# Kernel optimization log

Measured on AMD Instinct MI355X. Metric: run time of the kernel, lower is better.

The kernel has to match this reference:

```python
import jax, jax.numpy as jnp
import numpy as np
from jax import lax

NUM_LAYERS = 8
K = 3
C = 128  # residual/gate/skip channels
DIL_H = (1, 2, 4, 8, 1, 2, 4, 8)
DIL_W = (1, 2, 4, 8, 16, 32, 64, 128)
DN = ('NCHW', 'OIHW', 'NCHW')


def _conv(x, w, b, dh=1, dw=1, pad_h=0, pad_w=0):
    # causal along H: pad only on top by pad_h (equivalent to pytorch's
    # symmetric pad + out[:, :, :-pad_h] slice); symmetric along W.
    out = lax.conv_general_dilated(
        x, w, window_strides=(1, 1),
        padding=((pad_h, 0), (pad_w, pad_w)),
        rhs_dilation=(dh, dw), dimension_numbers=DN)
    return out + b[None, :, None, None]


def setup_inputs() -> dict:
    key = jax.random.key(0)
    ks = jax.random.split(key, 6)
    B, H, W = 2, 16, 4096
    return {
        'x': jax.random.normal(ks[0], (B, 1, H, W), jnp.float32),
        'c': jax.random.normal(ks[1], (B, 80, H, W), jnp.float32),
        'front_w': jax.random.normal(ks[2], (C, 1, 1, 1), jnp.float32),
        'front_b': jnp.zeros((C,), jnp.float32),
        'fg_w': jax.random.normal(ks[3], (NUM_LAYERS, 2 * C, C, K, K), jnp.float32) * (1.0 / np.sqrt(C * K * K)),
        'fg_b': jnp.zeros((NUM_LAYERS, 2 * C), jnp.float32),
        'fgc_w': jax.random.normal(ks[4], (NUM_LAYERS, 2 * C, 80, 1, 1), jnp.float32) * (1.0 / np.sqrt(80)),
        'fgc_b': jnp.zeros((NUM_LAYERS, 2 * C), jnp.float32),
        'rs_w': jax.random.normal(ks[5], (NUM_LAYERS, 2 * C, C, 1, 1), jnp.float32) * (1.0 / np.sqrt(C)),
        'rs_b': jnp.zeros((NUM_LAYERS, 2 * C), jnp.float32),
    }


def reference(x, c, front_w, front_b, fg_w, fg_b, fgc_w, fgc_b, rs_w, rs_b):
    # front 1x1 conv (causal but pad_h = 0 for kernel_size=1)
    h = _conv(x, front_w, front_b)  # [B, C, H, W]
    skip = jnp.zeros_like(h)
    for i in range(NUM_LAYERS):
        dh, dw = DIL_H[i], DIL_W[i]
        pad_h = dh * (K - 1)
        pad_w = dw * (K - 1) // 2
        # dilated causal conv -> [B, 2C, H, W]
        hg = _conv(h, fg_w[i], fg_b[i], dh, dw, pad_h, pad_w)
        # 1x1 conditioning conv on c
        cg = _conv(c, fgc_w[i], fgc_b[i])
        a = hg + cg
        acts = jnp.tanh(a[:, :C]) * jax.nn.sigmoid(a[:, C:])
        # 1x1 res/skip conv -> [B, 2C, H, W]
        rs = _conv(acts, rs_w[i], rs_b[i])
        h = h + rs[:, :C]
        skip = skip + rs[:, C:]
    return skip
```

## Files before the change

kernel.cpp:

```cpp
#include <hip/hip_runtime.h>
#include <math.h>

#define NL    8
#define CCH   128
#define CINC  80
#define CPAD  128
#define HH    16
#define WW    4096
#define HW    (HH*WW)
#define PADW  128
#define WWP   (WW + 2*PADW)
#define NT    10
#define PADF  64

#define HBF_N   (2*HH*WWP*CCH)
#define ZROW_N  (WWP*CCH)
#define CT_N    (2*HW*CPAD)
#define SKB_N   (2*HW*CCH)
#define GW_N    (NL*NT*4*16*64*8)
#define RW_N    (NL*4*16*64*8)

using v8s   = __attribute__((ext_vector_type(8))) short;
using f32x4 = __attribute__((ext_vector_type(4))) float;

__device__ __forceinline__ unsigned short f2bf(float f) {
    unsigned int u = __builtin_bit_cast(unsigned int, f);
    u += 0x7fffu + ((u >> 16) & 1u);
    return (unsigned short)(u >> 16);
}
__device__ __forceinline__ float bfu2f(unsigned int v) {
    return __builtin_bit_cast(float, v << 16);
}
__device__ __forceinline__ float gated(float a, float g) {
    float ac = fminf(a, 15.0f);
    float e  = __expf(2.0f * ac);
    float th = (e - 1.0f) * __builtin_amdgcn_rcpf(e + 1.0f);
    float sg = __builtin_amdgcn_rcpf(1.0f + __expf(-g));
    return th * sg;
}

__device__ __forceinline__ void gl_lds16(const void* g, void* l) {
    __builtin_amdgcn_global_load_lds(
        (const __attribute__((address_space(1))) unsigned int*)g,
        (__attribute__((address_space(3))) unsigned int*)l, 16, 0, 0);
}

__device__ __host__ __forceinline__ int tap_of(int t) { return (t < 7) ? t : (t == 8 ? 8 : 7); }

__global__ void prep_weights(const float* __restrict__ fg_w, const float* __restrict__ fgc_w,
                             const float* __restrict__ rs_w,
                             const float* __restrict__ fg_b, const float* __restrict__ fgc_b,
                             const float* __restrict__ rs_b,
                             unsigned short* __restrict__ gw, unsigned short* __restrict__ rw,
                             float* __restrict__ gbias, float* __restrict__ rbias) {
    const int total = GW_N + RW_N + 2 * NL * 256;
    const int stride = gridDim.x * blockDim.x;
    for (int idx = blockIdx.x * blockDim.x + threadIdx.x; idx < total; idx += stride) {
        if (idx < GW_N) {
            int t0 = idx;
            int j = t0 & 7;  t0 >>= 3;
            int l = t0 & 63; t0 >>= 6;
            int mt = t0 & 15; t0 >>= 4;
            int tq = t0 % (NT*4);
            int i  = t0 / (NT*4);
            int t  = tq >> 2, q = tq & 3;
            int m  = mt*16 + (l & 15);
            int oo = (m & 1)*128 + (m >> 1);
            int ci = q*32 + 8*(l >> 4) + j;
            float v;
            if (t == 7) {
                v = (ci < CINC) ? fgc_w[((size_t)i*256 + oo)*CINC + ci] : 0.0f;
            } else {
                int tt = tap_of(t);
                v = fg_w[(((size_t)i*256 + oo)*128 + ci)*9 + tt];
            }
            gw[idx] = f2bf(v);
        } else if (idx < GW_N + RW_N) {
            int t0 = idx - GW_N;
            int j = t0 & 7;  t0 >>= 3;
            int l = t0 & 63; t0 >>= 6;
            int mt = t0 & 15; t0 >>= 4;
            int q = t0 & 3;
            int i = t0 >> 2;
            int m  = mt*16 + (l & 15);
            int oo = (m & 1)*128 + (m >> 1);
            int ci = q*32 + 8*(l >> 4) + j;
            rw[idx - GW_N] = f2bf(rs_w[((size_t)i*256 + oo)*128 + ci]);
        } else {
            int t0 = idx - GW_N - RW_N;
            if (t0 < NL*256) {
                int i = t0 >> 8, m = t0 & 255;
                int oo = (m & 1)*128 + (m >> 1);
                gbias[t0] = fg_b[i*256 + oo] + fgc_b[i*256 + oo];
            } else {
                t0 -= NL*256;
                int i = t0 >> 8, m = t0 & 255;
                int oo = (m & 1)*128 + (m >> 1);
                rbias[t0] = rs_b[i*256 + oo];
            }
        }
    }
}

__global__ void front_kernel(const float* __restrict__ xsrc,
                             const float* __restrict__ fw, const float* __restrict__ fb,
                             unsigned short* __restrict__ hbf0,
                             unsigned short* __restrict__ hbf1, unsigned short* __restrict__ zrow) {
    const int stride = gridDim.x * blockDim.x;
    const int t0 = blockIdx.x * blockDim.x + threadIdx.x;
    for (int idx = t0; idx < HBF_N; idx += stride) {
        int c = idx & 127;
        int rest = idx >> 7;
        int xp = rest % WWP; rest /= WWP;
        int y = rest & 15;
        int b = rest >> 4;
        int x = xp - PADW;
        if (x >= 0 && x < WW)
            hbf0[idx] = f2bf(fw[c] * xsrc[((size_t)(b*HH + y))*WW + x] + fb[c]);
        else
            hbf0[idx] = 0;
    }
    const int PADN = 2*HH*2*PADW*CCH;
    for (int idx = t0; idx < PADN; idx += stride) {
        int c = idx & 127;
        int r = idx >> 7;
        int xo = r % (2*PADW); r /= (2*PADW);
        int y = r & 15;
        int b = r >> 4;
        int xp = (xo < PADW) ? xo : xo + WW;
        hbf1[(((size_t)(b*HH + y))*WWP + xp)*CCH + c] = 0;
    }
    for (int idx = t0; idx < ZROW_N; idx += stride) zrow[idx] = 0;
}

__global__ __launch_bounds__(256) void cond_transpose(const float* __restrict__ cin,
                                                      unsigned short* __restrict__ cT) {
    __shared__ unsigned short lt[CINC][72];
    const int tid = threadIdx.x, lane = tid & 63, w = tid >> 6;
    const int x0 = blockIdx.x * 64, y = blockIdx.y, b = blockIdx.z;
#pragma unroll
    for (int r = 0; r < 20; ++r) {
        int ci = w*20 + r;
        float v = cin[(((size_t)(b*CINC + ci))*HH + y)*WW + x0 + lane];
        lt[ci][lane] = f2bf(v);
    }
    __syncthreads();
    const int px = tid & 63, cg = tid >> 6;
    unsigned int pk[16];
#pragma unroll
    for (int kk = 0; kk < 16; ++kk) {
        int c0 = cg*32 + kk*2;
        unsigned int lo = (c0     < CINC) ? lt[c0][px]     : 0;
        unsigned int hi = (c0 + 1 < CINC) ? lt[c0 + 1][px] : 0;
        pk[kk] = lo | (hi << 16);
    }
    unsigned short* dst = cT + (((size_t)(b*HH + y))*WW + x0 + px)*CPAD + cg*32;
#pragma unroll
    for (int u = 0; u < 4; ++u)
        *(uint4*)(dst + u*8) = make_uint4(pk[u*4], pk[u*4+1], pk[u*4+2], pk[u*4+3]);
}

__global__ __launch_bounds__(256, 4) void layer_fused(
        const unsigned short* __restrict__ hin, unsigned short* __restrict__ hout,
        const unsigned short* __restrict__ zrow, const unsigned short* __restrict__ cT,
        const unsigned short* __restrict__ gw, const float* __restrict__ gbias,
        const unsigned short* __restrict__ rw, const float* __restrict__ rbias,
        unsigned short* __restrict__ skipbf, float* __restrict__ outp,
        int layer, int dh, int dw, int first) {
    __shared__ char sbuf[3 * 16384];

    const int tid = threadIdx.x, lane = tid & 63, w = tid >> 6;
    const int lrow = lane & 15, lk = lane >> 4;

    const int lin = blockIdx.x + 64*(blockIdx.y + 16*blockIdx.z);
    const int logical = (lin & 7)*256 + (lin >> 3);
    const int x0 = (logical & 63) * 64;
    const int y  = (logical >> 6) & 15;
    const int b  = logical >> 10;

    f32x4 acc[4][4];
#pragma unroll
    for (int mf = 0; mf < 4; ++mf)
#pragma unroll
        for (int nf = 0; nf < 4; ++nf) acc[mf][nf] = (f32x4){0.f, 0.f, 0.f, 0.f};

    const unsigned short* rowb[3];
#pragma unroll
    for (int kh = 0; kh < 3; ++kh) {
        int yin = y - (2 - kh)*dh;
        rowb[kh] = (yin >= 0) ? hin + ((size_t)(b*HH + yin))*WWP*CCH : zrow;
    }
    const char* cb = (const char*)(cT + (((size_t)(b*HH + y))*WW + x0)*CPAD);
    const unsigned short* gwl = gw + (((size_t)layer*NT*4*16) + w*4)*512 + lane*8;

    auto stage = [&](char* dst, const char* src) {
#pragma unroll
        for (int s = 0; s < 4; ++s) {
            unsigned o = (unsigned)(w*4 + s)*1024 + (unsigned)lane*16;
            unsigned g = o ^ (((o >> 8) & 7) << 4);
            gl_lds16(src + g, dst + (w*4 + s)*1024);
        }
    };
    auto stage_t = [&](int t) {
        const char* src;
        if (t == 7) src = cb;
        else {
            int tt = tap_of(t);
            int kh = tt / 3, kw = tt - kh*3;
            src = (const char*)(rowb[kh] + (size_t)(x0 + (kw - 1)*dw + PADW)*CCH);
        }
        stage(sbuf + (t % 3)*16384, src);
    };
    auto dsread = [&](const char* bb, int q, v8s (&bv)[4]) {
#pragma unroll
        for (int nf = 0; nf < 4; ++nf) {
            int px = nf*16 + lrow;
            int o = px*256 + ((q*64 + lk*16) ^ ((lrow & 7) << 4));
            bv[nf] = *(const v8s*)(bb + o);
        }
    };
    auto loadA = [&](int t, int q, v8s (&av)[4]) {
        const unsigned short* gq = gwl + (size_t)(t*4 + q)*16*512;
#pragma unroll
        for (int mf = 0; mf < 4; ++mf) av[mf] = *(const v8s*)(gq + mf*512);
    };
    auto mf16 = [&](v8s (&av)[4], v8s (&bv)[4]) {
        __builtin_amdgcn_s_setprio(1);
#pragma unroll
        for (int mf = 0; mf < 4; ++mf)
#pragma unroll
            for (int nf = 0; nf < 4; ++nf)
                acc[mf][nf] = __builtin_amdgcn_mfma_f32_16x16x32_bf16(av[mf], bv[nf], acc[mf][nf], 0, 0, 0);
        __builtin_amdgcn_s_setprio(0);
    };

    v8s aA[4], aB[4], bv[4];
    stage_t(0);
    stage_t(1);
    loadA(0, 0, aA);
    loadA(0, 1, aB);
#pragma unroll
    for (int t = 0; t < NT; ++t) {
        if (t == 0)      asm volatile("s_waitcnt vmcnt(12)" ::: "memory");
        else if (t == 1) asm volatile("s_waitcnt vmcnt(28)" ::: "memory");
        else             asm volatile("s_waitcnt vmcnt(36)" ::: "memory");
        __builtin_amdgcn_sched_barrier(0);
        __builtin_amdgcn_s_barrier();
        __builtin_amdgcn_sched_barrier(0);
        if (t + 2 < NT) stage_t(t + 2);
        const char* bb = sbuf + (t % 3)*16384;
        dsread(bb, 0, bv); mf16(aA, bv); loadA(t, 2, aA);
        dsread(bb, 1, bv); mf16(aB, bv); loadA(t, 3, aB);
        dsread(bb, 2, bv); mf16(aA, bv); if (t + 1 < NT) loadA(t + 1, 0, aA);
        dsread(bb, 3, bv); mf16(aB, bv); if (t + 1 < NT) loadA(t + 1, 1, aB);
    }

    char* sact = sbuf + 16384;
    const float* gb = gbias + layer*256;
#pragma unroll
    for (int mf = 0; mf < 4; ++mf) {
        int m0 = w*64 + mf*16 + lk*4;
        int c0 = m0 >> 1;
        float bF0 = gb[m0], bG0 = gb[m0+1], bF1 = gb[m0+2], bG1 = gb[m0+3];
#pragma unroll
        for (int nf = 0; nf < 4; ++nf) {
            int px = nf*16 + lrow;
            float o0 = gated(acc[mf][nf][0] + bF0, acc[mf][nf][1] + bG0);
            float o1 = gated(acc[mf][nf][2] + bF1, acc[mf][nf][3] + bG1);
            unsigned int pk = (unsigned int)f2bf(o0) | ((unsigned int)f2bf(o1) << 16);
            int byte = px*256 + c0*2;
            byte ^= (px & 7) << 4;
            *(unsigned int*)(sact + byte) = pk;
        }
    }
#pragma unroll
    for (int mf = 0; mf < 4; ++mf)
#pragma unroll
        for (int nf = 0; nf < 4; ++nf) acc[mf][nf] = (f32x4){0.f, 0.f, 0.f, 0.f};
    __syncthreads();

    const unsigned short* rwl = rw + (((size_t)layer*4*16) + w*4)*512 + lane*8;
#pragma unroll
    for (int q = 0; q < 4; ++q) {
        v8s av[4];
#pragma unroll
        for (int mf = 0; mf < 4; ++mf) av[mf] = *(const v8s*)(rwl + (size_t)(q*16 + mf)*512);
        dsread(sact, q, bv);
        __builtin_amdgcn_s_setprio(1);
#pragma unroll
        for (int mf = 0; mf < 4; ++mf)
#pragma unroll
            for (int nf = 0; nf < 4; ++nf)
                acc[mf][nf] = __builtin_amdgcn_mfma_f32_16x16x32_bf16(av[mf], bv[nf], acc[mf][nf], 0, 0, 0);
        __builtin_amdgcn_s_setprio(0);
    }

    unsigned int hold[4][4];
    if (layer < NL - 1) {
#pragma unroll
        for (int mf = 0; mf < 4; ++mf) {
            int c0 = w*32 + mf*8 + lk*2;
#pragma unroll
            for (int nf = 0; nf < 4; ++nf) {
                int px = nf*16 + lrow;
                int o = px*256 + ((c0*2) ^ ((px & 7) << 4));
                hold[mf][nf] = *(const unsigned int*)(sbuf + o);
            }
        }
    }
    __syncthreads();

    float* sresf = (float*)(sbuf + 16384);
    const int cp = tid >> 4, xg = tid & 15;
    const int pxl = tid & 63, cg = tid >> 6;

    if (layer < NL - 1) {
#pragma unroll
        for (int mf = 0; mf < 4; ++mf) {
            int c0 = w*32 + mf*8 + lk*2;
            float bR0 = rbias[layer*256 + 2*c0];
            float bR1 = rbias[layer*256 + 2*(c0 + 1)];
#pragma unroll
            for (int nf = 0; nf < 4; ++nf) {
                int px = nf*16 + lrow;
                float h0 = bfu2f(hold[mf][nf] & 0xffffu);
                float h1 = __builtin_bit_cast(float, hold[mf][nf] & 0xffff0000u);
                sresf[(c0    )*PADF + px] = h0 + acc[mf][nf][0] + bR0;
                sresf[(c0 + 1)*PADF + px] = h1 + acc[mf][nf][2] + bR1;
            }
        }
        __syncthreads();
        {
            unsigned int pk3[16];
#pragma unroll
            for (int j = 0; j < 16; ++j) {
                float lo = sresf[(cg*32 + 2*j    )*PADF + pxl];
                float hi = sresf[(cg*32 + 2*j + 1)*PADF + pxl];
                pk3[j] = (unsigned int)f2bf(lo) | ((unsigned int)f2bf(hi) << 16);
            }
            unsigned short* hrow = hout + (((size_t)(b*HH + y))*WWP + x0 + pxl + PADW)*CCH + cg*32;
#pragma unroll
            for (int u = 0; u < 4; ++u)
                *(uint4*)(hrow + u*8) = make_uint4(pk3[u*4], pk3[u*4+1], pk3[u*4+2], pk3[u*4+3]);
        }
        __syncthreads();
    }

#pragma unroll
    for (int mf = 0; mf < 4; ++mf) {
        int c0 = w*32 + mf*8 + lk*2;
#pragma unroll
        for (int nf = 0; nf < 4; ++nf) {
            int px = nf*16 + lrow;
            sresf[(c0    )*PADF + px] = acc[mf][nf][1];
            sresf[(c0 + 1)*PADF + px] = acc[mf][nf][3];
        }
    }
    __syncthreads();
#pragma unroll
    for (int it = 0; it < 8; ++it) {
        int cc = it*16 + cp;
        float4 s = *(float4*)(sresf + cc*PADF + xg*4);
        float bb2 = rbias[layer*256 + 2*cc + 1];
        s.x += bb2; s.y += bb2; s.z += bb2; s.w += bb2;
        size_t p = (((size_t)(b*CCH + cc))*HH + y)*WW + x0 + xg*4;
        if (layer == NL - 1) {
            uint2 o = *(const uint2*)(skipbf + p);
            float4 r;
            r.x = s.x + bfu2f(o.x & 0xffffu);
            r.y = s.y + bfu2f(o.x >> 16);
            r.z = s.z + bfu2f(o.y & 0xffffu);
            r.w = s.w + bfu2f(o.y >> 16);
            *(float4*)(outp + p) = r;
        } else {
            if (!first) {
                uint2 o = *(const uint2*)(skipbf + p);
                s.x += bfu2f(o.x & 0xffffu);
                s.y += bfu2f(o.x >> 16);
                s.z += bfu2f(o.y & 0xffffu);
                s.w += bfu2f(o.y >> 16);
            }
            uint2 np;
            np.x = (unsigned int)f2bf(s.x) | ((unsigned int)f2bf(s.y) << 16);
            np.y = (unsigned int)f2bf(s.z) | ((unsigned int)f2bf(s.w) << 16);
            *(uint2*)(skipbf + p) = np;
        }
    }
}

extern "C" void kernel_launch(void* const* d_in, const int* in_sizes, int n_in,
                              void* d_out, int out_size, void* d_ws, size_t ws_size,
                              hipStream_t stream) {
    const float* x       = (const float*)d_in[0];
    const float* c       = (const float*)d_in[1];
    const float* front_w = (const float*)d_in[2];
    const float* front_b = (const float*)d_in[3];
    const float* fg_w    = (const float*)d_in[4];
    const float* fg_b    = (const float*)d_in[5];
    const float* fgc_w   = (const float*)d_in[6];
    const float* fgc_b   = (const float*)d_in[7];
    const float* rs_w    = (const float*)d_in[8];
    const float* rs_b    = (const float*)d_in[9];

    char* ws = (char*)d_ws;
    unsigned short* hbf0 = (unsigned short*)ws;     ws += (size_t)HBF_N * 2;
    unsigned short* hbf1 = (unsigned short*)ws;     ws += (size_t)HBF_N * 2;
    unsigned short* zrow = (unsigned short*)ws;     ws += (size_t)ZROW_N * 2;
    unsigned short* cT   = (unsigned short*)ws;     ws += (size_t)CT_N * 2;
    unsigned short* skbf = (unsigned short*)ws;     ws += (size_t)SKB_N * 2;
    unsigned short* gw   = (unsigned short*)ws;     ws += (size_t)GW_N * 2;
    unsigned short* rwq  = (unsigned short*)ws;     ws += (size_t)RW_N * 2;
    float* gbias  = (float*)ws;                     ws += (size_t)NL * 256 * 4;
    float* rbias  = (float*)ws;

    float* outp = (float*)d_out;

    prep_weights<<<2048, 256, 0, stream>>>(fg_w, fgc_w, rs_w, fg_b, fgc_b, rs_b,
                                           gw, rwq, gbias, rbias);
    front_kernel<<<2048, 256, 0, stream>>>(x, front_w, front_b, hbf0, hbf1, zrow);
    cond_transpose<<<dim3(64, 16, 2), 256, 0, stream>>>(c, cT);

    static const int DILH[NL] = {1, 2, 4, 8, 1, 2, 4, 8};
    static const int DILW[NL] = {1, 2, 4, 8, 16, 32, 64, 128};

    for (int i = 0; i < NL; ++i) {
        const unsigned short* hin = (i & 1) ? hbf1 : hbf0;
        unsigned short*       hout= (i & 1) ? hbf0 : hbf1;
        layer_fused<<<dim3(64, 16, 2), 256, 0, stream>>>(hin, hout, zrow, cT, gw, gbias,
                                                         rwq, rbias, skbf, outp,
                                                         i, DILH[i], DILW[i], i == 0 ? 1 : 0);
    }
}
```

Baseline: 912.2 us.

## Add dedicated producer wavefront for LDS staging in layer kernel

Launches 320 threads per block so a fifth wavefront handles all global-to-LDS staging of the input tiles, while the four compute wavefronts only load weights and run MFMAs. This is warp specialization: it is meant to take the async-copy issue and vmcnt waits off the MFMA waves. In exchange the single producer issues four times as many copies per stage and still synchronizes at every tap barrier. The extra wave also sits idle through the epilogue and uses occupancy and registers.

New measurement: 1.848 ms. 103% more time.

```diff
diff --git a/kernel.cpp b/kernel.cpp
--- a/kernel.cpp
+++ b/kernel.cpp
@@ -160,7 +160,7 @@
         *(uint4*)(dst + u*8) = make_uint4(pk[u*4], pk[u*4+1], pk[u*4+2], pk[u*4+3]);
 }
 
-__global__ __launch_bounds__(256, 4) void layer_fused(
+__global__ __launch_bounds__(320, 4) void layer_fused(
         const unsigned short* __restrict__ hin, unsigned short* __restrict__ hout,
         const unsigned short* __restrict__ zrow, const unsigned short* __restrict__ cT,
         const unsigned short* __restrict__ gw, const float* __restrict__ gbias,
@@ -171,6 +171,7 @@
 
     const int tid = threadIdx.x, lane = tid & 63, w = tid >> 6;
     const int lrow = lane & 15, lk = lane >> 4;
+    const bool producer = (tid >= 256);
 
     const int lin = blockIdx.x + 64*(blockIdx.y + 16*blockIdx.z);
     const int logical = (lin & 7)*256 + (lin >> 3);
@@ -193,15 +194,7 @@
     const char* cb = (const char*)(cT + (((size_t)(b*HH + y))*WW + x0)*CPAD);
     const unsigned short* gwl = gw + (((size_t)layer*NT*4*16) + w*4)*512 + lane*8;
 
-    auto stage = [&](char* dst, const char* src) {
-#pragma unroll
-        for (int s = 0; s < 4; ++s) {
-            unsigned o = (unsigned)(w*4 + s)*1024 + (unsigned)lane*16;
-            unsigned g = o ^ (((o >> 8) & 7) << 4);
-            gl_lds16(src + g, dst + (w*4 + s)*1024);
-        }
-    };
-    auto stage_t = [&](int t) {
+    auto stage_p = [&](int t) {
         const char* src;
         if (t == 7) src = cb;
         else {
@@ -209,7 +202,13 @@
             int kh = tt / 3, kw = tt - kh*3;
             src = (const char*)(rowb[kh] + (size_t)(x0 + (kw - 1)*dw + PADW)*CCH);
         }
-        stage(sbuf + (t % 3)*16384, src);
+        char* dst = sbuf + (t % 3)*16384;
+#pragma unroll
+        for (int s = 0; s < 16; ++s) {
+            unsigned o = (unsigned)s*1024 + (unsigned)lane*16;
+            unsigned g = o ^ (((o >> 8) & 7) << 4);
+            gl_lds16(src + g, dst + s*1024);
+        }
     };
     auto dsread = [&](const char* bb, int q, v8s (&bv)[4]) {
 #pragma unroll
@@ -235,76 +234,86 @@
     };
 
     v8s aA[4], aB[4], bv[4];
-    stage_t(0);
-    stage_t(1);
-    loadA(0, 0, aA);
-    loadA(0, 1, aB);
+    if (producer) {
+        stage_p(0);
+        stage_p(1);
+    } else {
+        loadA(0, 0, aA);
+        loadA(0, 1, aB);
+    }
 #pragma unroll
     for (int t = 0; t < NT; ++t) {
-        if (t == 0)      asm volatile("s_waitcnt vmcnt(12)" ::: "memory");
-        else if (t == 1) asm volatile("s_waitcnt vmcnt(28)" ::: "memory");
-        else             asm volatile("s_waitcnt vmcnt(36)" ::: "memory");
+        if (producer) {
+            if (t < NT - 1) asm volatile("s_waitcnt vmcnt(16)" ::: "memory");
+            else            asm volatile("s_waitcnt vmcnt(0)" ::: "memory");
+        }
         __builtin_amdgcn_sched_barrier(0);
         __builtin_amdgcn_s_barrier();
         __builtin_amdgcn_sched_barrier(0);
-        if (t + 2 < NT) stage_t(t + 2);
-        const char* bb = sbuf + (t % 3)*16384;
-        dsread(bb, 0, bv); mf16(aA, bv); loadA(t, 2, aA);
-        dsread(bb, 1, bv); mf16(aB, bv); loadA(t, 3, aB);
-        dsread(bb, 2, bv); mf16(aA, bv); if (t + 1 < NT) loadA(t + 1, 0, aA);
-        dsread(bb, 3, bv); mf16(aB, bv); if (t + 1 < NT) loadA(t + 1, 1, aB);
+        if (producer) {
+            if (t + 2 < NT) stage_p(t + 2);
+        } else {
+            const char* bb = sbuf + (t % 3)*16384;
+            dsread(bb, 0, bv); mf16(aA, bv); loadA(t, 2, aA);
+            dsread(bb, 1, bv); mf16(aB, bv); loadA(t, 3, aB);
+            dsread(bb, 2, bv); mf16(aA, bv); if (t + 1 < NT) loadA(t + 1, 0, aA);
+            dsread(bb, 3, bv); mf16(aB, bv); if (t + 1 < NT) loadA(t + 1, 1, aB);
+        }
     }
 
     char* sact = sbuf + 16384;
-    const float* gb = gbias + layer*256;
-#pragma unroll
-    for (int mf = 0; mf < 4; ++mf) {
-        int m0 = w*64 + mf*16 + lk*4;
-        int c0 = m0 >> 1;
-        float bF0 = gb[m0], bG0 = gb[m0+1], bF1 = gb[m0+2], bG1 = gb[m0+3];
-#pragma unroll
-        for (int nf = 0; nf < 4; ++nf) {
-            int px = nf*16 + lrow;
-            float o0 = gated(acc[mf][nf][0] + bF0, acc[mf][nf][1] + bG0);
-            float o1 = gated(acc[mf][nf][2] + bF1, acc[mf][nf][3] + bG1);
-            unsigned int pk = (unsigned int)f2bf(o0) | ((unsigned int)f2bf(o1) << 16);
-            int byte = px*256 + c0*2;
-            byte ^= (px & 7) << 4;
-            *(unsigned int*)(sact + byte) = pk;
-        }
-    }
-#pragma unroll
-    for (int mf = 0; mf < 4; ++mf)
-#pragma unroll
-        for (int nf = 0; nf < 4; ++nf) acc[mf][nf] = (f32x4){0.f, 0.f, 0.f, 0.f};
-    __syncthreads();
-
-    const unsigned short* rwl = rw + (((size_t)layer*4*16) + w*4)*512 + lane*8;
-#pragma unroll
-    for (int q = 0; q < 4; ++q) {
-        v8s av[4];
-#pragma unroll
-        for (int mf = 0; mf < 4; ++mf) av[mf] = *(const v8s*)(rwl + (size_t)(q*16 + mf)*512);
-        dsread(sact, q, bv);
-        __builtin_amdgcn_s_setprio(1);
-#pragma unroll
-        for (int mf = 0; mf < 4; ++mf)
-#pragma unroll
-            for (int nf = 0; nf < 4; ++nf)
-                acc[mf][nf] = __builtin_amdgcn_mfma_f32_16x16x32_bf16(av[mf], bv[nf], acc[mf][nf], 0, 0, 0);
-        __builtin_amdgcn_s_setprio(0);
-    }
-
-    unsigned int hold[4][4];
-    if (layer < NL - 1) {
+    if (!producer) {
+        const float* gb = gbias + layer*256;
 #pragma unroll
         for (int mf = 0; mf < 4; ++mf) {
-            int c0 = w*32 + mf*8 + lk*2;
+            int m0 = w*64 + mf*16 + lk*4;
+            int c0 = m0 >> 1;
+            float bF0 = gb[m0], bG0 = gb[m0+1], bF1 = gb[m0+2], bG1 = gb[m0+3];
 #pragma unroll
             for (int nf = 0; nf < 4; ++nf) {
                 int px = nf*16 + lrow;
-                int o = px*256 + ((c0*2) ^ ((px & 7) << 4));
-                hold[mf][nf] = *(const unsigned int*)(sbuf + o);
+                float o0 = gated(acc[mf][nf][0] + bF0, acc[mf][nf][1] + bG0);
+                float o1 = gated(acc[mf][nf][2] + bF1, acc[mf][nf][3] + bG1);
+                unsigned int pk = (unsigned int)f2bf(o0) | ((unsigned int)f2bf(o1) << 16);
+                int byte = px*256 + c0*2;
+                byte ^= (px & 7) << 4;
+                *(unsigned int*)(sact + byte) = pk;
+            }
+        }
+#pragma unroll
+        for (int mf = 0; mf < 4; ++mf)
+#pragma unroll
+            for (int nf = 0; nf < 4; ++nf) acc[mf][nf] = (f32x4){0.f, 0.f, 0.f, 0.f};
+    }
+    __syncthreads();
+
+    unsigned int hold[4][4];
+    if (!producer) {
+        const unsigned short* rwl = rw + (((size_t)layer*4*16) + w*4)*512 + lane*8;
+#pragma unroll
+        for (int q = 0; q < 4; ++q) {
+            v8s av[4];
+#pragma unroll
+            for (int mf = 0; mf < 4; ++mf) av[mf] = *(const v8s*)(rwl + (size_t)(q*16 + mf)*512);
+            dsread(sact, q, bv);
+            __builtin_amdgcn_s_setprio(1);
+#pragma unroll
+            for (int mf = 0; mf < 4; ++mf)
+#pragma unroll
+                for (int nf = 0; nf < 4; ++nf)
+                    acc[mf][nf] = __builtin_amdgcn_mfma_f32_16x16x32_bf16(av[mf], bv[nf], acc[mf][nf], 0, 0, 0);
+            __builtin_amdgcn_s_setprio(0);
+        }
+        if (layer < NL - 1) {
+#pragma unroll
+            for (int mf = 0; mf < 4; ++mf) {
+                int c0 = w*32 + mf*8 + lk*2;
+#pragma unroll
+                for (int nf = 0; nf < 4; ++nf) {
+                    int px = nf*16 + lrow;
+                    int o = px*256 + ((c0*2) ^ ((px & 7) << 4));
+                    hold[mf][nf] = *(const unsigned int*)(sbuf + o);
+                }
             }
         }
     }
@@ -315,22 +324,24 @@
     const int pxl = tid & 63, cg = tid >> 6;
 
     if (layer < NL - 1) {
-#pragma unroll
-        for (int mf = 0; mf < 4; ++mf) {
-            int c0 = w*32 + mf*8 + lk*2;
-            float bR0 = rbias[layer*256 + 2*c0];
-            float bR1 = rbias[layer*256 + 2*(c0 + 1)];
-#pragma unroll
-            for (int nf = 0; nf < 4; ++nf) {
-                int px = nf*16 + lrow;
-                float h0 = bfu2f(hold[mf][nf] & 0xffffu);
-                float h1 = __builtin_bit_cast(float, hold[mf][nf] & 0xffff0000u);
-                sresf[(c0    )*PADF + px] = h0 + acc[mf][nf][0] + bR0;
-                sresf[(c0 + 1)*PADF + px] = h1 + acc[mf][nf][2] + bR1;
+        if (!producer) {
+#pragma unroll
+            for (int mf = 0; mf < 4; ++mf) {
+                int c0 = w*32 + mf*8 + lk*2;
+                float bR0 = rbias[layer*256 + 2*c0];
+                float bR1 = rbias[layer*256 + 2*(c0 + 1)];
+#pragma unroll
+                for (int nf = 0; nf < 4; ++nf) {
+                    int px = nf*16 + lrow;
+                    float h0 = bfu2f(hold[mf][nf] & 0xffffu);
+                    float h1 = __builtin_bit_cast(float, hold[mf][nf] & 0xffff0000u);
+                    sresf[(c0    )*PADF + px] = h0 + acc[mf][nf][0] + bR0;
+                    sresf[(c0 + 1)*PADF + px] = h1 + acc[mf][nf][2] + bR1;
+                }
             }
         }
         __syncthreads();
-        {
+        if (!producer) {
             unsigned int pk3[16];
 #pragma unroll
             for (int j = 0; j < 16; ++j) {
@@ -346,44 +357,48 @@
         __syncthreads();
     }
 
-#pragma unroll
-    for (int mf = 0; mf < 4; ++mf) {
-        int c0 = w*32 + mf*8 + lk*2;
-#pragma unroll
-        for (int nf = 0; nf < 4; ++nf) {
-            int px = nf*16 + lrow;
-            sresf[(c0    )*PADF + px] = acc[mf][nf][1];
-            sresf[(c0 + 1)*PADF + px] = acc[mf][nf][3];
+    if (!producer) {
+#pragma unroll
+        for (int mf = 0; mf < 4; ++mf) {
+            int c0 = w*32 + mf*8 + lk*2;
+#pragma unroll
+            for (int nf = 0; nf < 4; ++nf) {
+                int px = nf*16 + lrow;
+                sresf[(c0    )*PADF + px] = acc[mf][nf][1];
+                sresf[(c0 + 1)*PADF + px] = acc[mf][nf][3];
+            }
         }
     }
     __syncthreads();
-#pragma unroll
-    for (int it = 0; it < 8; ++it) {
-        int cc = it*16 + cp;
-        float4 s = *(float4*)(sresf + cc*PADF + xg*4);
-        float bb2 = rbias[layer*256 + 2*cc + 1];
-        s.x += bb2; s.y += bb2; s.z += bb2; s.w += bb2;
-        size_t p = (((size_t)(b*CCH + cc))*HH + y)*WW + x0 + xg*4;
-        if (layer == NL - 1) {
-            uint2 o = *(const uint2*)(skipbf + p);
-            float4 r;
-            r.x = s.x + bfu2f(o.x & 0xffffu);
-            r.y = s.y + bfu2f(o.x >> 16);
-            r.z = s.z + bfu2f(o.y & 0xffffu);
-            r.w = s.w + bfu2f(o.y >> 16);
-            *(float4*)(outp + p) = r;
-        } else {
-            if (!first) {
+    if (!producer) {
+#pragma unroll
+        for (int it = 0; it < 8; ++it) {
+            int cc = it*16 + cp;
+            float4 s = *(float4*)(sresf + cc*PADF + xg*4);
+            float bb2 = rbias[layer*256 + 2*cc + 1];
+            s.x += bb2; s.y += bb2; s.z += bb2; s.w += bb2;
+            size_t p = (((size_t)(b*CCH + cc))*HH + y)*WW + x0 + xg*4;
+            if (layer == NL - 1) {
                 uint2 o = *(const uint2*)(skipbf + p);
-                s.x += bfu2f(o.x & 0xffffu);
-                s.y += bfu2f(o.x >> 16);
-                s.z += bfu2f(o.y & 0xffffu);
-                s.w += bfu2f(o.y >> 16);
-            }
-            uint2 np;
-            np.x = (unsigned int)f2bf(s.x) | ((unsigned int)f2bf(s.y) << 16);
-            np.y = (unsigned int)f2bf(s.z) | ((unsigned int)f2bf(s.w) << 16);
-            *(uint2*)(skipbf + p) = np;
+                float4 r;
+                r.x = s.x + bfu2f(o.x & 0xffffu);
+                r.y = s.y + bfu2f(o.x >> 16);
+                r.z = s.z + bfu2f(o.y & 0xffffu);
+                r.w = s.w + bfu2f(o.y >> 16);
+                *(float4*)(outp + p) = r;
+            } else {
+                if (!first) {
+                    uint2 o = *(const uint2*)(skipbf + p);
+                    s.x += bfu2f(o.x & 0xffffu);
+                    s.y += bfu2f(o.x >> 16);
+                    s.z += bfu2f(o.y & 0xffffu);
+                    s.w += bfu2f(o.y >> 16);
+                }
+                uint2 np;
+                np.x = (unsigned int)f2bf(s.x) | ((unsigned int)f2bf(s.y) << 16);
+                np.y = (unsigned int)f2bf(s.z) | ((unsigned int)f2bf(s.w) << 16);
+                *(uint2*)(skipbf + p) = np;
+            }
         }
     }
 }
@@ -426,7 +441,7 @@
     for (int i = 0; i < NL; ++i) {
         const unsigned short* hin = (i & 1) ? hbf1 : hbf0;
         unsigned short*       hout= (i & 1) ? hbf0 : hbf1;
-        layer_fused<<<dim3(64, 16, 2), 256, 0, stream>>>(hin, hout, zrow, cT, gw, gbias,
+        layer_fused<<<dim3(64, 16, 2), 320, 0, stream>>>(hin, hout, zrow, cT, gw, gbias,
                                                          rwq, rbias, skbf, outp,
                                                          i, DILH[i], DILW[i], i == 0 ? 1 : 0);
     }
```
